# Kernel tuning notes

Measured on AMD Instinct MI355X. Metric: run time of the kernel, lower is better.

## Reference

```python
import jax, jax.numpy as jnp
import numpy as np
import math

ALPHA, BETA = 0.0, 0.1  # MarketRelation defaults


def setup_inputs() -> dict:
    key = jax.random.key(0)
    ks = jax.random.split(key, 15)
    n, T, d, K, C = 1024, 8, 64, 8, 64
    h = d  # hidden = (2*infeat)//2 = infeat
    s = 0.1
    u = jax.random.uniform(ks[13], (n, n, K), jnp.float32, 1e-6, 1.0 - 1e-6)
    return {
        "x":   jax.random.normal(ks[0], (n, T, d), jnp.float32),
        "Ind": jax.random.uniform(ks[1], (n, n), jnp.float32),
        "Loc": jax.random.uniform(ks[2], (n, n), jnp.float32),
        "a":   jax.random.normal(ks[3], (T, 1), jnp.float32),
        "W1m": jax.random.normal(ks[4], (2 * d, h), jnp.float32) * s,
        "b1m": jax.random.normal(ks[5], (h,), jnp.float32) * s,
        "W2m": jax.random.normal(ks[6], (h, 1), jnp.float32) * s,
        "b2m": jax.random.normal(ks[7], (1,), jnp.float32) * s,
        "W1s": jax.random.normal(ks[8], (2 * d, h), jnp.float32) * s,
        "b1s": jax.random.normal(ks[9], (h,), jnp.float32) * s,
        "W2s": jax.random.normal(ks[10], (h, K), jnp.float32) * s,
        "b2s": jax.random.normal(ks[11], (K,), jnp.float32) * s,
        "E":   jax.random.normal(ks[12], (K, n, C), jnp.float32) * s,
        "g":   -jnp.log(-jnp.log(u)),  # Gumbel(0,1) noise for gumbel_softmax
    }


def reference(x, Ind, Loc, a, W1m, b1m, W2m, b2m, W1s, b1s, W2s, b2s, E, g):
    n, T, d = x.shape
    # --- MarketRelation ---
    # fc1(concat(x_j, x_k)) == x_j @ W1m[:d] + x_k @ W1m[d:] + b1m (same math,
    # avoids materializing the N x N x 2d concat tensor)
    W1a, W1b = W1m[:d], W1m[d:]
    a_soft = jax.nn.softmax(a, axis=0)  # [T,1]
    A_mkt = jnp.zeros((n, n), x.dtype)
    for i in range(T):
        xi = x[:, i, :]                      # [n,d]
        hA = xi @ W1a                        # [n,h]
        hB = xi @ W1b                        # [n,h]
        hmat = jax.nn.relu(hA[:, None, :] + hB[None, :, :] + b1m)  # [n,n,h]
        adj = jax.nn.relu(hmat @ W2m + b2m)[..., 0]                # [n,n]
        factor = 1.0 + ALPHA * math.exp(-BETA * (T - i - 1))
        A_mkt = A_mkt + adj * (a_soft[i, 0] * factor)
    # --- NobsRelation (on last timestep) ---
    xl = x[:, -1, :]
    Ws1a, Ws1b = W1s[:d], W1s[d:]
    hs = jax.nn.relu((xl @ Ws1a)[:, None, :] + (xl @ Ws1b)[None, :, :] + b1s)
    logits = jax.nn.relu(hs @ W2s + b2s)          # [n,n,K]
    y = jax.nn.softmax(logits + g, axis=-1)       # gumbel_softmax, tau=1, soft
    D = jnp.einsum('knc,kmc->nmk', E, E)          # stack of E_k E_k^T, [n,n,K]
    A_nobs = jnp.sum(D * y, axis=-1)              # [n,n]
    return jnp.stack([Ind, Loc, A_mkt, A_nobs])   # [4,n,n]
```

## Files before the change

kernel.cpp:

```cpp
#include <hip/hip_runtime.h>

typedef unsigned short USH;
typedef float v2f __attribute__((ext_vector_type(2)));

__device__ __forceinline__ float bf2f(USH u) {
    return __uint_as_float(((unsigned int)u) << 16);
}
__device__ __forceinline__ float lo16(unsigned int u) { return __uint_as_float(u << 16); }
__device__ __forceinline__ float hi16(unsigned int u) { return __uint_as_float(u & 0xFFFF0000u); }
__device__ __forceinline__ USH f2bf(float f) {
    unsigned int i = __float_as_uint(f);
    i += 0x7FFFu + ((i >> 16) & 1u);
    return (USH)(i >> 16);
}
__device__ __forceinline__ v2f relu2(v2f s) {
    return __builtin_elementwise_max(s, (v2f)(0.0f));
}

__device__ __forceinline__ float ldf(const void* p, long idx, int bf) {
    return bf ? bf2f(((const USH*)p)[idx]) : ((const float*)p)[idx];
}
__device__ __forceinline__ void ld4(const void* p, long idx, int bf, float o[4]) {
    if (bf) {
        ushort4 u = *(const ushort4*)((const USH*)p + idx);
        o[0] = bf2f(u.x); o[1] = bf2f(u.y); o[2] = bf2f(u.z); o[3] = bf2f(u.w);
    } else {
        float4 v = *(const float4*)((const float*)p + idx);
        o[0] = v.x; o[1] = v.y; o[2] = v.z; o[3] = v.w;
    }
}

__device__ __forceinline__ int detect_bf(const void* ind) {
    const uint4* p = (const uint4*)ind;
    unsigned o = 0;
    #pragma unroll
    for (int i = 0; i < 8; ++i) { uint4 v = p[i]; o |= v.x | v.y | v.z | v.w; }
    return (o & 0x8000u) == 0;
}


__global__ __launch_bounds__(256) void k_pre_d(
    const void* __restrict__ x,
    const void* __restrict__ W1m,
    const void* __restrict__ b1m,
    const void* __restrict__ W1s,
    const void* __restrict__ b1s,
    const void* __restrict__ E,
    const void* __restrict__ IndDet,
    USH* __restrict__ hA, USH* __restrict__ hBb,
    USH* __restrict__ hsA, USH* __restrict__ hsBb,
    USH* __restrict__ D)
{
    __shared__ float smem[8192];
    float* sA = smem;
    float* sB = smem + 4096;
    const int bf = detect_bf(IndDet);
    const int tid = threadIdx.x;
    const int bid = blockIdx.x;
    const int tx = tid & 15, ty = tid >> 4;

    if (bid < 2048) {
        const int mb = (bid & 15) * 64, nb = ((bid >> 4) & 15) * 64, k = bid >> 8;
        const long ek = (long)k * 65536;
        {
            const int r_l = tid >> 2, cq = tid & 3;
            const long bn = ek + (long)(nb + r_l) * 64 + cq * 16;
            const long bm = ek + (long)(mb + r_l) * 64 + cq * 16;
            #pragma unroll
            for (int j = 0; j < 4; ++j) {
                const int c0 = cq * 16 + j * 4;
                float o[4];
                ld4(E, bn + j * 4, bf, o);
                #pragma unroll
                for (int e = 0; e < 4; ++e) sA[(c0 + e) * 64 + r_l] = o[e];
                ld4(E, bm + j * 4, bf, o);
                #pragma unroll
                for (int e = 0; e < 4; ++e) sB[(c0 + e) * 64 + r_l] = o[e];
            }
        }
        __syncthreads();
        const int m0 = tx * 4, n0 = ty * 4;
        v2f acc2[4][2] = {};
        #pragma unroll 8
        for (int c = 0; c < 64; ++c) {
            const float4 an = *(const float4*)&sA[c * 64 + n0];
            const float4 am = *(const float4*)&sB[c * 64 + m0];
            const float aa[4] = {an.x, an.y, an.z, an.w};
            v2f m01; m01.x = am.x; m01.y = am.y;
            v2f m23; m23.x = am.z; m23.y = am.w;
            #pragma unroll
            for (int ni = 0; ni < 4; ++ni) {
                const v2f av = (v2f)(aa[ni]);
                acc2[ni][0] = __builtin_elementwise_fma(av, m01, acc2[ni][0]);
                acc2[ni][1] = __builtin_elementwise_fma(av, m23, acc2[ni][1]);
            }
        }
        #pragma unroll
        for (int ni = 0; ni < 4; ++ni) {
            ushort4 o;
            o.x = f2bf(acc2[ni][0].x); o.y = f2bf(acc2[ni][0].y);
            o.z = f2bf(acc2[ni][1].x); o.w = f2bf(acc2[ni][1].y);
            *(ushort4*)&D[(long)k * 1048576 + (long)(nb + n0 + ni) * 1024 + mb + m0] = o;
        }
    } else {
        const int bid2 = bid - 2048;
        const int nbase = (bid2 & 15) * 64;
        const int by = bid2 >> 4;
        int t, rb;
        const void* Wsrc;
        const void* bias;
        USH* dst;
        if (by < 8)        { t = by;     rb = 0;  Wsrc = W1m; bias = nullptr; dst = hA + by * 65536; }
        else if (by < 16)  { t = by - 8; rb = 64; Wsrc = W1m; bias = b1m;     dst = hBb + (by - 8) * 65536; }
        else if (by == 16) { t = 7;      rb = 0;  Wsrc = W1s; bias = nullptr; dst = hsA; }
        else               { t = 7;      rb = 64; Wsrc = W1s; bias = b1s;     dst = hsBb; }

        {
            const int n_l = tid >> 2, dq = tid & 3;
            const long base = (long)(nbase + n_l) * 512 + t * 64 + dq * 16;
            #pragma unroll
            for (int j = 0; j < 4; ++j) {
                float o[4]; ld4(x, base + j * 4, bf, o);
                const int d0 = dq * 16 + j * 4;
                #pragma unroll
                for (int e = 0; e < 4; ++e) sA[(d0 + e) * 64 + n_l] = o[e];
            }
        }
        {
            const int d_l = tid >> 2, cq = tid & 3;
            const long base = (long)(rb + d_l) * 64 + cq * 16;
            #pragma unroll
            for (int j = 0; j < 4; ++j) {
                float o[4]; ld4(Wsrc, base + j * 4, bf, o);
                const int c0 = cq * 16 + j * 4;
                #pragma unroll
                for (int e = 0; e < 4; ++e) sB[d_l * 64 + c0 + e] = o[e];
            }
        }
        __syncthreads();

        const int c0 = tx * 4, nq = ty * 4;
        float acc[4][4] = {};
        #pragma unroll 16
        for (int d = 0; d < 64; ++d) {
            const float4 xa = *(const float4*)&sA[d * 64 + nq];
            const float4 wv = *(const float4*)&sB[d * 64 + c0];
            const float aa[4] = {xa.x, xa.y, xa.z, xa.w};
            const float ww[4] = {wv.x, wv.y, wv.z, wv.w};
            #pragma unroll
            for (int ci = 0; ci < 4; ++ci)
                #pragma unroll
                for (int ni = 0; ni < 4; ++ni)
                    acc[ci][ni] += ww[ci] * aa[ni];
        }
        #pragma unroll
        for (int ci = 0; ci < 4; ++ci) {
            const float bb = bias ? ldf(bias, c0 + ci, bf) : 0.0f;
            ushort4 o;
            o.x = f2bf(acc[ci][0] + bb); o.y = f2bf(acc[ci][1] + bb);
            o.z = f2bf(acc[ci][2] + bb); o.w = f2bf(acc[ci][3] + bb);
            *(ushort4*)&dst[(c0 + ci) * 1024 + nbase + nq] = o;
        }
    }
}

__global__ __launch_bounds__(256, 4) void k_main(
    const USH* __restrict__ hA, const USH* __restrict__ hBb,
    const USH* __restrict__ hsA, const USH* __restrict__ hsBb,
    const USH* __restrict__ Dm,
    const void* __restrict__ Ind, const void* __restrict__ Loc,
    const void* __restrict__ a, const void* __restrict__ W2m,
    const void* __restrict__ b2m, const void* __restrict__ W2s,
    const void* __restrict__ b2s, const void* __restrict__ g,
    void* __restrict__ out)
{
    __shared__ float As[2][64 * 32];
    __shared__ float Bs[2][64 * 32];
    __shared__ float w2s_l[64 * 8];
    __shared__ float w2m_l[64];
    __shared__ float asoft_l[8];

    const int bf = detect_bf(Ind);
    const int tid = threadIdx.x;
    const int mb = blockIdx.x * 32, nb = blockIdx.y * 32;
    const int tx = tid & 15, ty = tid >> 4;
    const int m0 = tx * 2, n0 = ty * 2;

    if (tid < 64) w2m_l[tid] = ldf(W2m, tid, bf);
    if (tid >= 64 && tid < 192) {
        const int q = tid - 64;
        float o[4]; ld4(W2s, q * 4, bf, o);
        #pragma unroll
        for (int e = 0; e < 4; ++e) w2s_l[q * 4 + e] = o[e];
    }
    if (tid < 8) {
        float av[8], mx = -1e30f, s = 0.0f;
        #pragma unroll
        for (int k = 0; k < 8; ++k) { av[k] = ldf(a, k, bf); mx = fmaxf(mx, av[k]); }
        #pragma unroll
        for (int k = 0; k < 8; ++k) s += __expf(av[k] - mx);
        asoft_l[tid] = __expf(av[tid] - mx) / s;
    }
    const float b2m_f = ldf(b2m, 0, bf);

    const int offA = (tid >> 2) * 1024 + nb + (tid & 3) * 8;
    const int offB = (tid >> 2) * 1024 + mb + (tid & 3) * 8;
    const int ldsOff = tid * 8;

    {
        const uint4 pa = *(const uint4*)(hA + offA);
        const uint4 pb = *(const uint4*)(hBb + offB);
        float4 fa0, fa1, fb0, fb1;
        fa0.x = lo16(pa.x); fa0.y = hi16(pa.x); fa0.z = lo16(pa.y); fa0.w = hi16(pa.y);
        fa1.x = lo16(pa.z); fa1.y = hi16(pa.z); fa1.z = lo16(pa.w); fa1.w = hi16(pa.w);
        fb0.x = lo16(pb.x); fb0.y = hi16(pb.x); fb0.z = lo16(pb.y); fb0.w = hi16(pb.y);
        fb1.x = lo16(pb.z); fb1.y = hi16(pb.z); fb1.z = lo16(pb.w); fb1.w = hi16(pb.w);
        *(float4*)&As[0][ldsOff] = fa0; *(float4*)&As[0][ldsOff + 4] = fa1;
        *(float4*)&Bs[0][ldsOff] = fb0; *(float4*)&Bs[0][ldsOff + 4] = fb1;
    }
    __syncthreads();

    v2f amk2[2] = {(v2f)(0.0f), (v2f)(0.0f)};

    for (int t = 0; t < 8; ++t) {
        const int cur = t & 1, nxt = cur ^ 1;
        const USH* srcA = (t < 7) ? (hA + (t + 1) * 65536) : hsA;
        const USH* srcB = (t < 7) ? (hBb + (t + 1) * 65536) : hsBb;
        const uint4 pa = *(const uint4*)(srcA + offA);
        const uint4 pb = *(const uint4*)(srcB + offB);

        v2f acc2[2] = {(v2f)(0.0f), (v2f)(0.0f)};
        #pragma unroll
        for (int c4 = 0; c4 < 16; ++c4) {
            const float4 wq = *(const float4*)&w2m_l[c4 * 4];
            const float ww[4] = {wq.x, wq.y, wq.z, wq.w};
            #pragma unroll
            for (int j = 0; j < 4; ++j) {
                const int c = c4 * 4 + j;
                const v2f aa = *(const v2f*)&As[cur][(c << 5) + n0];
                const v2f bb = *(const v2f*)&Bs[cur][(c << 5) + m0];
                const v2f wv = (v2f)(ww[j]);
                const v2f s0 = relu2((v2f)(aa.x) + bb);
                const v2f s1 = relu2((v2f)(aa.y) + bb);
                acc2[0] = __builtin_elementwise_fma(s0, wv, acc2[0]);
                acc2[1] = __builtin_elementwise_fma(s1, wv, acc2[1]);
            }
        }
        const v2f asv = (v2f)(asoft_l[t]);
        const v2f b2v = (v2f)(b2m_f);
        amk2[0] = __builtin_elementwise_fma(relu2(acc2[0] + b2v), asv, amk2[0]);
        amk2[1] = __builtin_elementwise_fma(relu2(acc2[1] + b2v), asv, amk2[1]);

        float4 f0, f1;
        f0.x = lo16(pa.x); f0.y = hi16(pa.x); f0.z = lo16(pa.y); f0.w = hi16(pa.y);
        f1.x = lo16(pa.z); f1.y = hi16(pa.z); f1.z = lo16(pa.w); f1.w = hi16(pa.w);
        *(float4*)&As[nxt][ldsOff] = f0; *(float4*)&As[nxt][ldsOff + 4] = f1;
        f0.x = lo16(pb.x); f0.y = hi16(pb.x); f0.z = lo16(pb.y); f0.w = hi16(pb.y);
        f1.x = lo16(pb.z); f1.y = hi16(pb.z); f1.z = lo16(pb.w); f1.w = hi16(pb.w);
        *(float4*)&Bs[nxt][ldsOff] = f0; *(float4*)&Bs[nxt][ldsOff + 4] = f1;
        __syncthreads();
    }

    v2f lgp[2][8];
    #pragma unroll
    for (int i = 0; i < 2; ++i)
        #pragma unroll
        for (int k = 0; k < 8; ++k) lgp[i][k] = (v2f)(0.0f);

    #pragma unroll 4
    for (int c = 0; c < 64; ++c) {
        const v2f aa = *(const v2f*)&As[0][(c << 5) + n0];
        const v2f bb = *(const v2f*)&Bs[0][(c << 5) + m0];
        const v2f z0 = relu2((v2f)(aa.x) + bb);
        const v2f z1 = relu2((v2f)(aa.y) + bb);
        const float4 wa = *(const float4*)&w2s_l[c << 3];
        const float4 wb = *(const float4*)&w2s_l[(c << 3) + 4];
        const float wk[8] = {wa.x, wa.y, wa.z, wa.w, wb.x, wb.y, wb.z, wb.w};
        #pragma unroll
        for (int k = 0; k < 8; ++k) {
            const v2f wkv = (v2f)(wk[k]);
            lgp[0][k] = __builtin_elementwise_fma(z0, wkv, lgp[0][k]);
            lgp[1][k] = __builtin_elementwise_fma(z1, wkv, lgp[1][k]);
        }
    }

    float b2s_f[8];
    #pragma unroll
    for (int k = 0; k < 8; ++k) b2s_f[k] = ldf(b2s, k, bf);

    #pragma unroll
    for (int i = 0; i < 2; ++i) {
        const long rowoff = (long)(nb + n0 + i) * 1024 + mb + m0;
        float gv[16];
        ld4(g, rowoff * 8 + 0, bf, gv + 0);
        ld4(g, rowoff * 8 + 4, bf, gv + 4);
        ld4(g, rowoff * 8 + 8, bf, gv + 8);
        ld4(g, rowoff * 8 + 12, bf, gv + 12);

        float s0 = 0.0f, s1 = 0.0f, d0 = 0.0f, d1 = 0.0f;
        #pragma unroll
        for (int k = 0; k < 8; ++k) {
            const v2f lr = relu2(lgp[i][k] + (v2f)(b2s_f[k]));
            const float e0 = __expf(lr.x + gv[k]);
            const float e1 = __expf(lr.y + gv[8 + k]);
            s0 += e0; s1 += e1;
            const ushort2 dv = *(const ushort2*)&Dm[((long)k << 20) + rowoff];
            d0 += bf2f(dv.x) * e0;
            d1 += bf2f(dv.y) * e1;
        }

        if (bf) {
            USH* o = (USH*)out;
            *(ushort2*)&o[rowoff] = *(const ushort2*)&((const USH*)Ind)[rowoff];
            *(ushort2*)&o[1048576 + rowoff] = *(const ushort2*)&((const USH*)Loc)[rowoff];
            ushort2 o2; o2.x = f2bf(amk2[i].x); o2.y = f2bf(amk2[i].y);
            *(ushort2*)&o[2 * 1048576 + rowoff] = o2;
            ushort2 o3; o3.x = f2bf(d0 / s0); o3.y = f2bf(d1 / s1);
            *(ushort2*)&o[3 * 1048576 + rowoff] = o3;
        } else {
            float* o = (float*)out;
            *(float2*)&o[rowoff] = *(const float2*)&((const float*)Ind)[rowoff];
            *(float2*)&o[1048576 + rowoff] = *(const float2*)&((const float*)Loc)[rowoff];
            float2 o2; o2.x = amk2[i].x; o2.y = amk2[i].y;
            *(float2*)&o[2 * 1048576 + rowoff] = o2;
            float2 o3; o3.x = d0 / s0; o3.y = d1 / s1;
            *(float2*)&o[3 * 1048576 + rowoff] = o3;
        }
    }
}

extern "C" void kernel_launch(void* const* d_in, const int* in_sizes, int n_in,
                              void* d_out, int out_size, void* d_ws, size_t ws_size,
                              hipStream_t stream) {
    const void* x   = d_in[0];
    const void* Ind = d_in[1];
    const void* Loc = d_in[2];
    const void* a   = d_in[3];
    const void* W1m = d_in[4];
    const void* b1m = d_in[5];
    const void* W2m = d_in[6];
    const void* b2m = d_in[7];
    const void* W1s = d_in[8];
    const void* b1s = d_in[9];
    const void* W2s = d_in[10];
    const void* b2s = d_in[11];
    const void* E   = d_in[12];
    const void* g   = d_in[13];

    USH* ws   = (USH*)d_ws;
    USH* hA   = ws;
    USH* hBb  = hA + 524288;
    USH* hsA  = hBb + 524288;
    USH* hsBb = hsA + 65536;
    USH* Dm   = hsBb + 65536;

    k_pre_d<<<dim3(2336), 256, 0, stream>>>(x, W1m, b1m, W1s, b1s, E, Ind,
                                            hA, hBb, hsA, hsBb, Dm);
    k_main<<<dim3(32, 32), 256, 0, stream>>>(hA, hBb, hsA, hsBb, Dm,
                                             Ind, Loc, a, W2m, b2m, W2s, b2s,
                                             g, d_out);
}
```

Measured before the change: 186.0 us.

## Restructure main kernel: fp32 intermediates, wave-uniform A rows, register W2m

The precomputed hidden projections are now stored as fp32 instead of bf16. hA is laid out row-major per node, so each wave reads its eight n-rows as wave-uniform (scalar/broadcast) loads. hB is stored channel-pair interleaved and staged in LDS, double-buffered across timesteps. The main kernel tile changes to 64 m by 32 n, with each lane owning one m column and eight n rows, and W2m and the softmax weights are held in registers. This removes bf16 unpacking and most LDS traffic for A, but doubles intermediate memory size, raises register pressure (launch bounds drop to 2 blocks per SM), and makes the output stores scalar per element.

```diff
diff --git a/kernel.cpp b/kernel.cpp
--- a/kernel.cpp
+++ b/kernel.cpp
@@ -6,8 +6,6 @@
 __device__ __forceinline__ float bf2f(USH u) {
     return __uint_as_float(((unsigned int)u) << 16);
 }
-__device__ __forceinline__ float lo16(unsigned int u) { return __uint_as_float(u << 16); }
-__device__ __forceinline__ float hi16(unsigned int u) { return __uint_as_float(u & 0xFFFF0000u); }
 __device__ __forceinline__ USH f2bf(float f) {
     unsigned int i = __float_as_uint(f);
     i += 0x7FFFu + ((i >> 16) & 1u);
@@ -47,8 +45,8 @@
     const void* __restrict__ b1s,
     const void* __restrict__ E,
     const void* __restrict__ IndDet,
-    USH* __restrict__ hA, USH* __restrict__ hBb,
-    USH* __restrict__ hsA, USH* __restrict__ hsBb,
+    float* __restrict__ hAf,
+    float* __restrict__ hBf,
     USH* __restrict__ D)
 {
     __shared__ float smem[8192];
@@ -109,11 +107,11 @@
         int t, rb;
         const void* Wsrc;
         const void* bias;
-        USH* dst;
-        if (by < 8)        { t = by;     rb = 0;  Wsrc = W1m; bias = nullptr; dst = hA + by * 65536; }
-        else if (by < 16)  { t = by - 8; rb = 64; Wsrc = W1m; bias = b1m;     dst = hBb + (by - 8) * 65536; }
-        else if (by == 16) { t = 7;      rb = 0;  Wsrc = W1s; bias = nullptr; dst = hsA; }
-        else               { t = 7;      rb = 64; Wsrc = W1s; bias = b1s;     dst = hsBb; }
+        float* dst;
+        if (by < 8)        { t = by;     rb = 0;  Wsrc = W1m; bias = nullptr; dst = hAf + by * 65536; }
+        else if (by < 16)  { t = by - 8; rb = 64; Wsrc = W1m; bias = b1m;     dst = hBf + (by - 8) * 65536; }
+        else if (by == 16) { t = 7;      rb = 0;  Wsrc = W1s; bias = nullptr; dst = hAf + 8 * 65536; }
+        else               { t = 7;      rb = 64; Wsrc = W1s; bias = b1s;     dst = hBf + 8 * 65536; }
 
         {
             const int n_l = tid >> 2, dq = tid & 3;
@@ -153,20 +151,32 @@
                 for (int ni = 0; ni < 4; ++ni)
                     acc[ci][ni] += ww[ci] * aa[ni];
         }
-        #pragma unroll
-        for (int ci = 0; ci < 4; ++ci) {
-            const float bb = bias ? ldf(bias, c0 + ci, bf) : 0.0f;
-            ushort4 o;
-            o.x = f2bf(acc[ci][0] + bb); o.y = f2bf(acc[ci][1] + bb);
-            o.z = f2bf(acc[ci][2] + bb); o.w = f2bf(acc[ci][3] + bb);
-            *(ushort4*)&dst[(c0 + ci) * 1024 + nbase + nq] = o;
-        }
-    }
-}
-
-__global__ __launch_bounds__(256, 4) void k_main(
-    const USH* __restrict__ hA, const USH* __restrict__ hBb,
-    const USH* __restrict__ hsA, const USH* __restrict__ hsBb,
+        if (rb == 0) {
+            #pragma unroll
+            for (int ni = 0; ni < 4; ++ni) {
+                float4 o;
+                o.x = acc[0][ni]; o.y = acc[1][ni]; o.z = acc[2][ni]; o.w = acc[3][ni];
+                *(float4*)&dst[(nbase + nq + ni) * 64 + c0] = o;
+            }
+        } else {
+            float b[4];
+            #pragma unroll
+            for (int ci = 0; ci < 4; ++ci) b[ci] = ldf(bias, c0 + ci, bf);
+            #pragma unroll
+            for (int ni = 0; ni < 4; ++ni) {
+                const int mr = nbase + nq + ni;
+                v2f o0; o0.x = acc[0][ni] + b[0]; o0.y = acc[1][ni] + b[1];
+                v2f o1; o1.x = acc[2][ni] + b[2]; o1.y = acc[3][ni] + b[3];
+                *(v2f*)&dst[(c0 >> 1) * 2048 + mr * 2] = o0;
+                *(v2f*)&dst[((c0 >> 1) + 1) * 2048 + mr * 2] = o1;
+            }
+        }
+    }
+}
+
+__global__ __launch_bounds__(256, 2) void k_main(
+    const float* __restrict__ hAf,
+    const float* __restrict__ hBf,
     const USH* __restrict__ Dm,
     const void* __restrict__ Ind, const void* __restrict__ Loc,
     const void* __restrict__ a, const void* __restrict__ W2m,
@@ -174,157 +184,169 @@
     const void* __restrict__ b2s, const void* __restrict__ g,
     void* __restrict__ out)
 {
-    __shared__ float As[2][64 * 32];
-    __shared__ float Bs[2][64 * 32];
-    __shared__ float w2s_l[64 * 8];
-    __shared__ float w2m_l[64];
-    __shared__ float asoft_l[8];
+    __shared__ float Bs[2][4096];
+    __shared__ float w2s_l[512];
 
     const int bf = detect_bf(Ind);
     const int tid = threadIdx.x;
-    const int mb = blockIdx.x * 32, nb = blockIdx.y * 32;
-    const int tx = tid & 15, ty = tid >> 4;
-    const int m0 = tx * 2, n0 = ty * 2;
-
-    if (tid < 64) w2m_l[tid] = ldf(W2m, tid, bf);
-    if (tid >= 64 && tid < 192) {
-        const int q = tid - 64;
-        float o[4]; ld4(W2s, q * 4, bf, o);
-        #pragma unroll
-        for (int e = 0; e < 4; ++e) w2s_l[q * 4 + e] = o[e];
-    }
-    if (tid < 8) {
+    const int mb = blockIdx.x * 64;
+    const int nb = blockIdx.y * 32;
+    const int lane = tid & 63;
+    const int wid = __builtin_amdgcn_readfirstlane(tid >> 6);
+    const int m = mb + lane;
+    const int scp = tid >> 5;
+    const int sq4 = (tid & 31) << 2;
+
+    #pragma unroll
+    for (int i = 0; i < 4; ++i) {
+        const int cp = i * 8 + scp;
+        const float4 v = *(const float4*)(hBf + cp * 2048 + mb * 2 + sq4);
+        *(float4*)&Bs[0][cp * 128 + sq4] = v;
+    }
+    if (tid < 128) {
+        float o[4];
+        ld4(W2s, tid * 4, bf, o);
+        w2s_l[tid * 4 + 0] = o[0]; w2s_l[tid * 4 + 1] = o[1];
+        w2s_l[tid * 4 + 2] = o[2]; w2s_l[tid * 4 + 3] = o[3];
+    }
+
+    v2f w2mv[32];
+    #pragma unroll
+    for (int q = 0; q < 16; ++q) {
+        float o[4]; ld4(W2m, q * 4, bf, o);
+        v2f u; u.x = o[0]; u.y = o[1]; w2mv[2 * q] = u;
+        v2f w; w.x = o[2]; w.y = o[3]; w2mv[2 * q + 1] = w;
+    }
+    const float b2m_f = ldf(b2m, 0, bf);
+    float asf[8];
+    {
         float av[8], mx = -1e30f, s = 0.0f;
         #pragma unroll
         for (int k = 0; k < 8; ++k) { av[k] = ldf(a, k, bf); mx = fmaxf(mx, av[k]); }
         #pragma unroll
-        for (int k = 0; k < 8; ++k) s += __expf(av[k] - mx);
-        asoft_l[tid] = __expf(av[tid] - mx) / s;
-    }
-    const float b2m_f = ldf(b2m, 0, bf);
-
-    const int offA = (tid >> 2) * 1024 + nb + (tid & 3) * 8;
-    const int offB = (tid >> 2) * 1024 + mb + (tid & 3) * 8;
-    const int ldsOff = tid * 8;
-
-    {
-        const uint4 pa = *(const uint4*)(hA + offA);
-        const uint4 pb = *(const uint4*)(hBb + offB);
-        float4 fa0, fa1, fb0, fb1;
-        fa0.x = lo16(pa.x); fa0.y = hi16(pa.x); fa0.z = lo16(pa.y); fa0.w = hi16(pa.y);
-        fa1.x = lo16(pa.z); fa1.y = hi16(pa.z); fa1.z = lo16(pa.w); fa1.w = hi16(pa.w);
-        fb0.x = lo16(pb.x); fb0.y = hi16(pb.x); fb0.z = lo16(pb.y); fb0.w = hi16(pb.y);
-        fb1.x = lo16(pb.z); fb1.y = hi16(pb.z); fb1.z = lo16(pb.w); fb1.w = hi16(pb.w);
-        *(float4*)&As[0][ldsOff] = fa0; *(float4*)&As[0][ldsOff + 4] = fa1;
-        *(float4*)&Bs[0][ldsOff] = fb0; *(float4*)&Bs[0][ldsOff + 4] = fb1;
+        for (int k = 0; k < 8; ++k) { av[k] = __expf(av[k] - mx); s += av[k]; }
+        #pragma unroll
+        for (int k = 0; k < 8; ++k) asf[k] = av[k] / s;
     }
     __syncthreads();
 
-    v2f amk2[2] = {(v2f)(0.0f), (v2f)(0.0f)};
+    float amk[8] = {0.f, 0.f, 0.f, 0.f, 0.f, 0.f, 0.f, 0.f};
 
     for (int t = 0; t < 8; ++t) {
-        const int cur = t & 1, nxt = cur ^ 1;
-        const USH* srcA = (t < 7) ? (hA + (t + 1) * 65536) : hsA;
-        const USH* srcB = (t < 7) ? (hBb + (t + 1) * 65536) : hsBb;
-        const uint4 pa = *(const uint4*)(srcA + offA);
-        const uint4 pb = *(const uint4*)(srcB + offB);
-
-        v2f acc2[2] = {(v2f)(0.0f), (v2f)(0.0f)};
-        #pragma unroll
-        for (int c4 = 0; c4 < 16; ++c4) {
-            const float4 wq = *(const float4*)&w2m_l[c4 * 4];
-            const float ww[4] = {wq.x, wq.y, wq.z, wq.w};
-            #pragma unroll
-            for (int j = 0; j < 4; ++j) {
-                const int c = c4 * 4 + j;
-                const v2f aa = *(const v2f*)&As[cur][(c << 5) + n0];
-                const v2f bb = *(const v2f*)&Bs[cur][(c << 5) + m0];
-                const v2f wv = (v2f)(ww[j]);
-                const v2f s0 = relu2((v2f)(aa.x) + bb);
-                const v2f s1 = relu2((v2f)(aa.y) + bb);
-                acc2[0] = __builtin_elementwise_fma(s0, wv, acc2[0]);
-                acc2[1] = __builtin_elementwise_fma(s1, wv, acc2[1]);
-            }
-        }
-        const v2f asv = (v2f)(asoft_l[t]);
-        const v2f b2v = (v2f)(b2m_f);
-        amk2[0] = __builtin_elementwise_fma(relu2(acc2[0] + b2v), asv, amk2[0]);
-        amk2[1] = __builtin_elementwise_fma(relu2(acc2[1] + b2v), asv, amk2[1]);
-
-        float4 f0, f1;
-        f0.x = lo16(pa.x); f0.y = hi16(pa.x); f0.z = lo16(pa.y); f0.w = hi16(pa.y);
-        f1.x = lo16(pa.z); f1.y = hi16(pa.z); f1.z = lo16(pa.w); f1.w = hi16(pa.w);
-        *(float4*)&As[nxt][ldsOff] = f0; *(float4*)&As[nxt][ldsOff + 4] = f1;
-        f0.x = lo16(pb.x); f0.y = hi16(pb.x); f0.z = lo16(pb.y); f0.w = hi16(pb.y);
-        f1.x = lo16(pb.z); f1.y = hi16(pb.z); f1.z = lo16(pb.w); f1.w = hi16(pb.w);
-        *(float4*)&Bs[nxt][ldsOff] = f0; *(float4*)&Bs[nxt][ldsOff + 4] = f1;
+        const int cur = t & 1;
+        float4 st[4];
+        #pragma unroll
+        for (int i = 0; i < 4; ++i) {
+            const int cp = i * 8 + scp;
+            st[i] = *(const float4*)(hBf + (t + 1) * 65536 + cp * 2048 + mb * 2 + sq4);
+        }
+
+        v2f acc[8];
+        #pragma unroll
+        for (int ni = 0; ni < 8; ++ni) acc[ni] = (v2f)(0.0f);
+        const float* At = hAf + ((t * 1024) + nb + wid * 8) * 64;
+        #pragma unroll
+        for (int ch = 0; ch < 4; ++ch) {
+            v2f bbv[8];
+            #pragma unroll
+            for (int j = 0; j < 8; ++j)
+                bbv[j] = *(const v2f*)&Bs[cur][(ch * 8 + j) * 128 + lane * 2];
+            #pragma unroll
+            for (int ni = 0; ni < 8; ++ni) {
+                const v2f* Ar = (const v2f*)(At + ni * 64 + ch * 16);
+                #pragma unroll
+                for (int j = 0; j < 8; ++j) {
+                    const v2f s = relu2(bbv[j] + Ar[j]);
+                    acc[ni] = __builtin_elementwise_fma(s, w2mv[ch * 8 + j], acc[ni]);
+                }
+            }
+        }
+        const float as_t = asf[t];
+        #pragma unroll
+        for (int ni = 0; ni < 8; ++ni)
+            amk[ni] += fmaxf(acc[ni].x + acc[ni].y + b2m_f, 0.0f) * as_t;
+
+        #pragma unroll
+        for (int i = 0; i < 4; ++i) {
+            const int cp = i * 8 + scp;
+            *(float4*)&Bs[cur ^ 1][cp * 128 + sq4] = st[i];
+        }
         __syncthreads();
     }
 
-    v2f lgp[2][8];
-    #pragma unroll
-    for (int i = 0; i < 2; ++i)
-        #pragma unroll
-        for (int k = 0; k < 8; ++k) lgp[i][k] = (v2f)(0.0f);
-
-    #pragma unroll 4
-    for (int c = 0; c < 64; ++c) {
-        const v2f aa = *(const v2f*)&As[0][(c << 5) + n0];
-        const v2f bb = *(const v2f*)&Bs[0][(c << 5) + m0];
-        const v2f z0 = relu2((v2f)(aa.x) + bb);
-        const v2f z1 = relu2((v2f)(aa.y) + bb);
-        const float4 wa = *(const float4*)&w2s_l[c << 3];
-        const float4 wb = *(const float4*)&w2s_l[(c << 3) + 4];
-        const float wk[8] = {wa.x, wa.y, wa.z, wa.w, wb.x, wb.y, wb.z, wb.w};
-        #pragma unroll
-        for (int k = 0; k < 8; ++k) {
-            const v2f wkv = (v2f)(wk[k]);
-            lgp[0][k] = __builtin_elementwise_fma(z0, wkv, lgp[0][k]);
-            lgp[1][k] = __builtin_elementwise_fma(z1, wkv, lgp[1][k]);
-        }
-    }
-
-    float b2s_f[8];
-    #pragma unroll
-    for (int k = 0; k < 8; ++k) b2s_f[k] = ldf(b2s, k, bf);
-
-    #pragma unroll
-    for (int i = 0; i < 2; ++i) {
-        const long rowoff = (long)(nb + n0 + i) * 1024 + mb + m0;
-        float gv[16];
-        ld4(g, rowoff * 8 + 0, bf, gv + 0);
+    v2f lg[8][4];
+    #pragma unroll
+    for (int ni = 0; ni < 8; ++ni)
+        #pragma unroll
+        for (int kp = 0; kp < 4; ++kp) lg[ni][kp] = (v2f)(0.0f);
+
+    const float* A8 = hAf + (8 * 1024 + nb + wid * 8) * 64;
+    #pragma unroll
+    for (int ch = 0; ch < 16; ++ch) {
+        const v2f bb0 = *(const v2f*)&Bs[0][(ch * 2 + 0) * 128 + lane * 2];
+        const v2f bb1 = *(const v2f*)&Bs[0][(ch * 2 + 1) * 128 + lane * 2];
+        v2f wsl[4][4];
+        #pragma unroll
+        for (int cc = 0; cc < 4; ++cc) {
+            const float4 wa = *(const float4*)&w2s_l[(ch * 4 + cc) * 8];
+            const float4 wb = *(const float4*)&w2s_l[(ch * 4 + cc) * 8 + 4];
+            wsl[cc][0].x = wa.x; wsl[cc][0].y = wa.y;
+            wsl[cc][1].x = wa.z; wsl[cc][1].y = wa.w;
+            wsl[cc][2].x = wb.x; wsl[cc][2].y = wb.y;
+            wsl[cc][3].x = wb.z; wsl[cc][3].y = wb.w;
+        }
+        #pragma unroll
+        for (int ni = 0; ni < 8; ++ni) {
+            const v2f* Ar = (const v2f*)(A8 + ni * 64 + ch * 4);
+            const v2f s0 = relu2(bb0 + Ar[0]);
+            const v2f s1 = relu2(bb1 + Ar[1]);
+            #pragma unroll
+            for (int kp = 0; kp < 4; ++kp) {
+                lg[ni][kp] = __builtin_elementwise_fma((v2f)(s0.x), wsl[0][kp], lg[ni][kp]);
+                lg[ni][kp] = __builtin_elementwise_fma((v2f)(s0.y), wsl[1][kp], lg[ni][kp]);
+                lg[ni][kp] = __builtin_elementwise_fma((v2f)(s1.x), wsl[2][kp], lg[ni][kp]);
+                lg[ni][kp] = __builtin_elementwise_fma((v2f)(s1.y), wsl[3][kp], lg[ni][kp]);
+            }
+        }
+    }
+
+    v2f b2sv[4];
+    #pragma unroll
+    for (int kp = 0; kp < 4; ++kp) {
+        b2sv[kp].x = ldf(b2s, 2 * kp, bf);
+        b2sv[kp].y = ldf(b2s, 2 * kp + 1, bf);
+    }
+
+    #pragma unroll
+    for (int ni = 0; ni < 8; ++ni) {
+        const int n = nb + wid * 8 + ni;
+        const long rowoff = ((long)n << 10) + m;
+        float gv[8];
+        ld4(g, rowoff * 8, bf, gv);
         ld4(g, rowoff * 8 + 4, bf, gv + 4);
-        ld4(g, rowoff * 8 + 8, bf, gv + 8);
-        ld4(g, rowoff * 8 + 12, bf, gv + 12);
-
-        float s0 = 0.0f, s1 = 0.0f, d0 = 0.0f, d1 = 0.0f;
-        #pragma unroll
-        for (int k = 0; k < 8; ++k) {
-            const v2f lr = relu2(lgp[i][k] + (v2f)(b2s_f[k]));
-            const float e0 = __expf(lr.x + gv[k]);
-            const float e1 = __expf(lr.y + gv[8 + k]);
-            s0 += e0; s1 += e1;
-            const ushort2 dv = *(const ushort2*)&Dm[((long)k << 20) + rowoff];
-            d0 += bf2f(dv.x) * e0;
-            d1 += bf2f(dv.y) * e1;
-        }
-
+        float ssum = 0.0f, dsum = 0.0f;
+        #pragma unroll
+        for (int kp = 0; kp < 4; ++kp) {
+            const v2f lr = relu2(lg[ni][kp] + b2sv[kp]);
+            const float e0 = __expf(lr.x + gv[2 * kp]);
+            const float e1 = __expf(lr.y + gv[2 * kp + 1]);
+            ssum += e0 + e1;
+            dsum += bf2f(Dm[((long)(2 * kp) << 20) + rowoff]) * e0
+                  + bf2f(Dm[((long)(2 * kp + 1) << 20) + rowoff]) * e1;
+        }
+        const float nobs = dsum / ssum;
         if (bf) {
             USH* o = (USH*)out;
-            *(ushort2*)&o[rowoff] = *(const ushort2*)&((const USH*)Ind)[rowoff];
-            *(ushort2*)&o[1048576 + rowoff] = *(const ushort2*)&((const USH*)Loc)[rowoff];
-            ushort2 o2; o2.x = f2bf(amk2[i].x); o2.y = f2bf(amk2[i].y);
-            *(ushort2*)&o[2 * 1048576 + rowoff] = o2;
-            ushort2 o3; o3.x = f2bf(d0 / s0); o3.y = f2bf(d1 / s1);
-            *(ushort2*)&o[3 * 1048576 + rowoff] = o3;
+            o[rowoff] = ((const USH*)Ind)[rowoff];
+            o[1048576 + rowoff] = ((const USH*)Loc)[rowoff];
+            o[2 * 1048576 + rowoff] = f2bf(amk[ni]);
+            o[3 * 1048576 + rowoff] = f2bf(nobs);
         } else {
             float* o = (float*)out;
-            *(float2*)&o[rowoff] = *(const float2*)&((const float*)Ind)[rowoff];
-            *(float2*)&o[1048576 + rowoff] = *(const float2*)&((const float*)Loc)[rowoff];
-            float2 o2; o2.x = amk2[i].x; o2.y = amk2[i].y;
-            *(float2*)&o[2 * 1048576 + rowoff] = o2;
-            float2 o3; o3.x = d0 / s0; o3.y = d1 / s1;
-            *(float2*)&o[3 * 1048576 + rowoff] = o3;
+            o[rowoff] = ((const float*)Ind)[rowoff];
+            o[1048576 + rowoff] = ((const float*)Loc)[rowoff];
+            o[2 * 1048576 + rowoff] = amk[ni];
+            o[3 * 1048576 + rowoff] = nobs;
         }
     }
 }
@@ -347,16 +369,14 @@
     const void* E   = d_in[12];
     const void* g   = d_in[13];
 
-    USH* ws   = (USH*)d_ws;
-    USH* hA   = ws;
-    USH* hBb  = hA + 524288;
-    USH* hsA  = hBb + 524288;
-    USH* hsBb = hsA + 65536;
-    USH* Dm   = hsBb + 65536;
+    float* ws  = (float*)d_ws;
+    float* hAf = ws;
+    float* hBf = hAf + 589824;
+    USH*   Dm  = (USH*)(hBf + 589824);
 
     k_pre_d<<<dim3(2336), 256, 0, stream>>>(x, W1m, b1m, W1s, b1s, E, Ind,
-                                            hA, hBb, hsA, hsBb, Dm);
-    k_main<<<dim3(32, 32), 256, 0, stream>>>(hA, hBb, hsA, hsBb, Dm,
+                                            hAf, hBf, Dm);
+    k_main<<<dim3(16, 32), 256, 0, stream>>>(hAf, hBf, Dm,
                                              Ind, Loc, a, W2m, b2m, W2s, b2s,
                                              g, d_out);
 }
```

Measured after the change: 510.3 us. 2.74x slower.

## Store hidden projections as fp32 and enlarge k_main tile to 64x32

Applied to the files above, without the earlier changes.

The precomputed hidden projections hA/hB are now stored as fp32 instead of bf16, with the NOBS projections packed as a ninth slice. This removes the unpack step in k_main and makes indexing uniform. k_main's per-block tile grows from 32x32 to 64x32, with each thread handling 4 rows instead of 2, so every loaded B value and weight is reused across more outputs. The costs are double the workspace traffic for the projections, more LDS, and higher register pressure, with launch_bounds lowered to 2 blocks per SM.

```diff
diff --git a/kernel.cpp b/kernel.cpp
--- a/kernel.cpp
+++ b/kernel.cpp
@@ -6,8 +6,6 @@
 __device__ __forceinline__ float bf2f(USH u) {
     return __uint_as_float(((unsigned int)u) << 16);
 }
-__device__ __forceinline__ float lo16(unsigned int u) { return __uint_as_float(u << 16); }
-__device__ __forceinline__ float hi16(unsigned int u) { return __uint_as_float(u & 0xFFFF0000u); }
 __device__ __forceinline__ USH f2bf(float f) {
     unsigned int i = __float_as_uint(f);
     i += 0x7FFFu + ((i >> 16) & 1u);
@@ -47,8 +45,8 @@
     const void* __restrict__ b1s,
     const void* __restrict__ E,
     const void* __restrict__ IndDet,
-    USH* __restrict__ hA, USH* __restrict__ hBb,
-    USH* __restrict__ hsA, USH* __restrict__ hsBb,
+    float* __restrict__ hAf,
+    float* __restrict__ hBf,
     USH* __restrict__ D)
 {
     __shared__ float smem[8192];
@@ -109,11 +107,11 @@
         int t, rb;
         const void* Wsrc;
         const void* bias;
-        USH* dst;
-        if (by < 8)        { t = by;     rb = 0;  Wsrc = W1m; bias = nullptr; dst = hA + by * 65536; }
-        else if (by < 16)  { t = by - 8; rb = 64; Wsrc = W1m; bias = b1m;     dst = hBb + (by - 8) * 65536; }
-        else if (by == 16) { t = 7;      rb = 0;  Wsrc = W1s; bias = nullptr; dst = hsA; }
-        else               { t = 7;      rb = 64; Wsrc = W1s; bias = b1s;     dst = hsBb; }
+        float* dst;
+        if (by < 8)        { t = by;     rb = 0;  Wsrc = W1m; bias = nullptr; dst = hAf + by * 65536; }
+        else if (by < 16)  { t = by - 8; rb = 64; Wsrc = W1m; bias = b1m;     dst = hBf + (by - 8) * 65536; }
+        else if (by == 16) { t = 7;      rb = 0;  Wsrc = W1s; bias = nullptr; dst = hAf + 8 * 65536; }
+        else               { t = 7;      rb = 64; Wsrc = W1s; bias = b1s;     dst = hBf + 8 * 65536; }
 
         {
             const int n_l = tid >> 2, dq = tid & 3;
@@ -153,20 +151,24 @@
                 for (int ni = 0; ni < 4; ++ni)
                     acc[ci][ni] += ww[ci] * aa[ni];
         }
+        float b[4] = {0.f, 0.f, 0.f, 0.f};
+        if (bias) {
+            #pragma unroll
+            for (int ci = 0; ci < 4; ++ci) b[ci] = ldf(bias, c0 + ci, bf);
+        }
         #pragma unroll
         for (int ci = 0; ci < 4; ++ci) {
-            const float bb = bias ? ldf(bias, c0 + ci, bf) : 0.0f;
-            ushort4 o;
-            o.x = f2bf(acc[ci][0] + bb); o.y = f2bf(acc[ci][1] + bb);
-            o.z = f2bf(acc[ci][2] + bb); o.w = f2bf(acc[ci][3] + bb);
-            *(ushort4*)&dst[(c0 + ci) * 1024 + nbase + nq] = o;
-        }
-    }
-}
-
-__global__ __launch_bounds__(256, 4) void k_main(
-    const USH* __restrict__ hA, const USH* __restrict__ hBb,
-    const USH* __restrict__ hsA, const USH* __restrict__ hsBb,
+            float4 o;
+            o.x = acc[ci][0] + b[ci]; o.y = acc[ci][1] + b[ci];
+            o.z = acc[ci][2] + b[ci]; o.w = acc[ci][3] + b[ci];
+            *(float4*)&dst[(c0 + ci) * 1024 + nbase + nq] = o;
+        }
+    }
+}
+
+__global__ __launch_bounds__(256, 2) void k_main(
+    const float* __restrict__ hAf,
+    const float* __restrict__ hBf,
     const USH* __restrict__ Dm,
     const void* __restrict__ Ind, const void* __restrict__ Loc,
     const void* __restrict__ a, const void* __restrict__ W2m,
@@ -174,17 +176,21 @@
     const void* __restrict__ b2s, const void* __restrict__ g,
     void* __restrict__ out)
 {
-    __shared__ float As[2][64 * 32];
-    __shared__ float Bs[2][64 * 32];
-    __shared__ float w2s_l[64 * 8];
+    __shared__ float As[2][4096];
+    __shared__ float Bs[2][2048];
+    __shared__ float w2s_l[512];
     __shared__ float w2m_l[64];
     __shared__ float asoft_l[8];
 
     const int bf = detect_bf(Ind);
     const int tid = threadIdx.x;
-    const int mb = blockIdx.x * 32, nb = blockIdx.y * 32;
+    const int mb = blockIdx.x * 32, nb = blockIdx.y * 64;
     const int tx = tid & 15, ty = tid >> 4;
-    const int m0 = tx * 2, n0 = ty * 2;
+    const int n0 = ty * 4;
+    const int m0 = tx * 2;
+
+    const int cA = tid >> 4, qA = (tid & 15) * 4;
+    const int cB = tid >> 3, qB = (tid & 7) * 4;
 
     if (tid < 64) w2m_l[tid] = ldf(W2m, tid, bf);
     if (tid >= 64 && tid < 192) {
@@ -203,94 +209,104 @@
     }
     const float b2m_f = ldf(b2m, 0, bf);
 
-    const int offA = (tid >> 2) * 1024 + nb + (tid & 3) * 8;
-    const int offB = (tid >> 2) * 1024 + mb + (tid & 3) * 8;
-    const int ldsOff = tid * 8;
-
-    {
-        const uint4 pa = *(const uint4*)(hA + offA);
-        const uint4 pb = *(const uint4*)(hBb + offB);
-        float4 fa0, fa1, fb0, fb1;
-        fa0.x = lo16(pa.x); fa0.y = hi16(pa.x); fa0.z = lo16(pa.y); fa0.w = hi16(pa.y);
-        fa1.x = lo16(pa.z); fa1.y = hi16(pa.z); fa1.z = lo16(pa.w); fa1.w = hi16(pa.w);
-        fb0.x = lo16(pb.x); fb0.y = hi16(pb.x); fb0.z = lo16(pb.y); fb0.w = hi16(pb.y);
-        fb1.x = lo16(pb.z); fb1.y = hi16(pb.z); fb1.z = lo16(pb.w); fb1.w = hi16(pb.w);
-        *(float4*)&As[0][ldsOff] = fa0; *(float4*)&As[0][ldsOff + 4] = fa1;
-        *(float4*)&Bs[0][ldsOff] = fb0; *(float4*)&Bs[0][ldsOff + 4] = fb1;
+    #pragma unroll
+    for (int p = 0; p < 4; ++p) {
+        const int c = cA + p * 16;
+        *(float4*)&As[0][c * 64 + qA] = *(const float4*)(hAf + (long)c * 1024 + nb + qA);
+    }
+    #pragma unroll
+    for (int p = 0; p < 2; ++p) {
+        const int c = cB + p * 32;
+        *(float4*)&Bs[0][c * 32 + qB] = *(const float4*)(hBf + (long)c * 1024 + mb + qB);
     }
     __syncthreads();
 
-    v2f amk2[2] = {(v2f)(0.0f), (v2f)(0.0f)};
+    v2f amk[4] = {(v2f)(0.0f), (v2f)(0.0f), (v2f)(0.0f), (v2f)(0.0f)};
 
     for (int t = 0; t < 8; ++t) {
         const int cur = t & 1, nxt = cur ^ 1;
-        const USH* srcA = (t < 7) ? (hA + (t + 1) * 65536) : hsA;
-        const USH* srcB = (t < 7) ? (hBb + (t + 1) * 65536) : hsBb;
-        const uint4 pa = *(const uint4*)(srcA + offA);
-        const uint4 pb = *(const uint4*)(srcB + offB);
-
-        v2f acc2[2] = {(v2f)(0.0f), (v2f)(0.0f)};
-        #pragma unroll
+        const float* srcA = hAf + (long)(t + 1) * 65536;
+        const float* srcB = hBf + (long)(t + 1) * 65536;
+        float4 pfa[4], pfb[2];
+        #pragma unroll
+        for (int p = 0; p < 4; ++p)
+            pfa[p] = *(const float4*)(srcA + (long)(cA + p * 16) * 1024 + nb + qA);
+        #pragma unroll
+        for (int p = 0; p < 2; ++p)
+            pfb[p] = *(const float4*)(srcB + (long)(cB + p * 32) * 1024 + mb + qB);
+
+        v2f acc[4] = {(v2f)(0.0f), (v2f)(0.0f), (v2f)(0.0f), (v2f)(0.0f)};
+        const float* Ac = As[cur];
+        const float* Bc = Bs[cur];
+        #pragma unroll 4
         for (int c4 = 0; c4 < 16; ++c4) {
             const float4 wq = *(const float4*)&w2m_l[c4 * 4];
             const float ww[4] = {wq.x, wq.y, wq.z, wq.w};
             #pragma unroll
             for (int j = 0; j < 4; ++j) {
                 const int c = c4 * 4 + j;
-                const v2f aa = *(const v2f*)&As[cur][(c << 5) + n0];
-                const v2f bb = *(const v2f*)&Bs[cur][(c << 5) + m0];
+                const float4 aq = *(const float4*)&Ac[c * 64 + n0];
+                const v2f bb = *(const v2f*)&Bc[c * 32 + m0];
+                const float aa[4] = {aq.x, aq.y, aq.z, aq.w};
                 const v2f wv = (v2f)(ww[j]);
-                const v2f s0 = relu2((v2f)(aa.x) + bb);
-                const v2f s1 = relu2((v2f)(aa.y) + bb);
-                acc2[0] = __builtin_elementwise_fma(s0, wv, acc2[0]);
-                acc2[1] = __builtin_elementwise_fma(s1, wv, acc2[1]);
+                #pragma unroll
+                for (int ni = 0; ni < 4; ++ni) {
+                    const v2f s = relu2(bb + (v2f)(aa[ni]));
+                    acc[ni] = __builtin_elementwise_fma(s, wv, acc[ni]);
+                }
             }
         }
         const v2f asv = (v2f)(asoft_l[t]);
         const v2f b2v = (v2f)(b2m_f);
-        amk2[0] = __builtin_elementwise_fma(relu2(acc2[0] + b2v), asv, amk2[0]);
-        amk2[1] = __builtin_elementwise_fma(relu2(acc2[1] + b2v), asv, amk2[1]);
-
-        float4 f0, f1;
-        f0.x = lo16(pa.x); f0.y = hi16(pa.x); f0.z = lo16(pa.y); f0.w = hi16(pa.y);
-        f1.x = lo16(pa.z); f1.y = hi16(pa.z); f1.z = lo16(pa.w); f1.w = hi16(pa.w);
-        *(float4*)&As[nxt][ldsOff] = f0; *(float4*)&As[nxt][ldsOff + 4] = f1;
-        f0.x = lo16(pb.x); f0.y = hi16(pb.x); f0.z = lo16(pb.y); f0.w = hi16(pb.y);
-        f1.x = lo16(pb.z); f1.y = hi16(pb.z); f1.z = lo16(pb.w); f1.w = hi16(pb.w);
-        *(float4*)&Bs[nxt][ldsOff] = f0; *(float4*)&Bs[nxt][ldsOff + 4] = f1;
+        #pragma unroll
+        for (int ni = 0; ni < 4; ++ni)
+            amk[ni] = __builtin_elementwise_fma(relu2(acc[ni] + b2v), asv, amk[ni]);
+
+        #pragma unroll
+        for (int p = 0; p < 4; ++p)
+            *(float4*)&As[nxt][(cA + p * 16) * 64 + qA] = pfa[p];
+        #pragma unroll
+        for (int p = 0; p < 2; ++p)
+            *(float4*)&Bs[nxt][(cB + p * 32) * 32 + qB] = pfb[p];
         __syncthreads();
     }
 
-    v2f lgp[2][8];
-    #pragma unroll
-    for (int i = 0; i < 2; ++i)
-        #pragma unroll
-        for (int k = 0; k < 8; ++k) lgp[i][k] = (v2f)(0.0f);
-
-    #pragma unroll 4
-    for (int c = 0; c < 64; ++c) {
-        const v2f aa = *(const v2f*)&As[0][(c << 5) + n0];
-        const v2f bb = *(const v2f*)&Bs[0][(c << 5) + m0];
-        const v2f z0 = relu2((v2f)(aa.x) + bb);
-        const v2f z1 = relu2((v2f)(aa.y) + bb);
-        const float4 wa = *(const float4*)&w2s_l[c << 3];
-        const float4 wb = *(const float4*)&w2s_l[(c << 3) + 4];
-        const float wk[8] = {wa.x, wa.y, wa.z, wa.w, wb.x, wb.y, wb.z, wb.w};
-        #pragma unroll
-        for (int k = 0; k < 8; ++k) {
-            const v2f wkv = (v2f)(wk[k]);
-            lgp[0][k] = __builtin_elementwise_fma(z0, wkv, lgp[0][k]);
-            lgp[1][k] = __builtin_elementwise_fma(z1, wkv, lgp[1][k]);
-        }
-    }
-
-    float b2s_f[8];
-    #pragma unroll
-    for (int k = 0; k < 8; ++k) b2s_f[k] = ldf(b2s, k, bf);
-
-    #pragma unroll
-    for (int i = 0; i < 2; ++i) {
-        const long rowoff = (long)(nb + n0 + i) * 1024 + mb + m0;
+    v2f lgm[4][8];
+    #pragma unroll
+    for (int ni = 0; ni < 4; ++ni)
+        #pragma unroll
+        for (int k = 0; k < 8; ++k) lgm[ni][k] = (v2f)(0.0f);
+
+    #pragma unroll 2
+    for (int c4 = 0; c4 < 16; ++c4) {
+        #pragma unroll
+        for (int j = 0; j < 4; ++j) {
+            const int c = c4 * 4 + j;
+            const float4 aq = *(const float4*)&As[0][c * 64 + n0];
+            const v2f bb = *(const v2f*)&Bs[0][c * 32 + m0];
+            const float aa[4] = {aq.x, aq.y, aq.z, aq.w};
+            const float4 wa = *(const float4*)&w2s_l[c * 8];
+            const float4 wb = *(const float4*)&w2s_l[c * 8 + 4];
+            const float wk[8] = {wa.x, wa.y, wa.z, wa.w, wb.x, wb.y, wb.z, wb.w};
+            #pragma unroll
+            for (int ni = 0; ni < 4; ++ni) {
+                const v2f z = relu2(bb + (v2f)(aa[ni]));
+                #pragma unroll
+                for (int k = 0; k < 8; ++k)
+                    lgm[ni][k] = __builtin_elementwise_fma(z, (v2f)(wk[k]), lgm[ni][k]);
+            }
+        }
+    }
+
+    float b2sv[8];
+    #pragma unroll
+    for (int k = 0; k < 8; ++k) b2sv[k] = ldf(b2s, k, bf);
+
+    const int mg = mb + m0;
+    #pragma unroll
+    for (int ni = 0; ni < 4; ++ni) {
+        const int n = nb + n0 + ni;
+        const long rowoff = ((long)n << 10) + mg;
         float gv[16];
         ld4(g, rowoff * 8 + 0, bf, gv + 0);
         ld4(g, rowoff * 8 + 4, bf, gv + 4);
@@ -300,7 +316,7 @@
         float s0 = 0.0f, s1 = 0.0f, d0 = 0.0f, d1 = 0.0f;
         #pragma unroll
         for (int k = 0; k < 8; ++k) {
-            const v2f lr = relu2(lgp[i][k] + (v2f)(b2s_f[k]));
+            const v2f lr = relu2(lgm[ni][k] + (v2f)(b2sv[k]));
             const float e0 = __expf(lr.x + gv[k]);
             const float e1 = __expf(lr.y + gv[8 + k]);
             s0 += e0; s1 += e1;
@@ -313,7 +329,7 @@
             USH* o = (USH*)out;
             *(ushort2*)&o[rowoff] = *(const ushort2*)&((const USH*)Ind)[rowoff];
             *(ushort2*)&o[1048576 + rowoff] = *(const ushort2*)&((const USH*)Loc)[rowoff];
-            ushort2 o2; o2.x = f2bf(amk2[i].x); o2.y = f2bf(amk2[i].y);
+            ushort2 o2; o2.x = f2bf(amk[ni].x); o2.y = f2bf(amk[ni].y);
             *(ushort2*)&o[2 * 1048576 + rowoff] = o2;
             ushort2 o3; o3.x = f2bf(d0 / s0); o3.y = f2bf(d1 / s1);
             *(ushort2*)&o[3 * 1048576 + rowoff] = o3;
@@ -321,7 +337,7 @@
             float* o = (float*)out;
             *(float2*)&o[rowoff] = *(const float2*)&((const float*)Ind)[rowoff];
             *(float2*)&o[1048576 + rowoff] = *(const float2*)&((const float*)Loc)[rowoff];
-            float2 o2; o2.x = amk2[i].x; o2.y = amk2[i].y;
+            float2 o2; o2.x = amk[ni].x; o2.y = amk[ni].y;
             *(float2*)&o[2 * 1048576 + rowoff] = o2;
             float2 o3; o3.x = d0 / s0; o3.y = d1 / s1;
             *(float2*)&o[3 * 1048576 + rowoff] = o3;
@@ -347,16 +363,14 @@
     const void* E   = d_in[12];
     const void* g   = d_in[13];
 
-    USH* ws   = (USH*)d_ws;
-    USH* hA   = ws;
-    USH* hBb  = hA + 524288;
-    USH* hsA  = hBb + 524288;
-    USH* hsBb = hsA + 65536;
-    USH* Dm   = hsBb + 65536;
+    float* ws  = (float*)d_ws;
+    float* hAf = ws;
+    float* hBf = hAf + 589824;
+    USH*   Dm  = (USH*)(hBf + 589824);
 
     k_pre_d<<<dim3(2336), 256, 0, stream>>>(x, W1m, b1m, W1s, b1s, E, Ind,
-                                            hA, hBb, hsA, hsBb, Dm);
-    k_main<<<dim3(32, 32), 256, 0, stream>>>(hA, hBb, hsA, hsBb, Dm,
+                                            hAf, hBf, Dm);
+    k_main<<<dim3(32, 16), 256, 0, stream>>>(hAf, hBf, Dm,
                                              Ind, Loc, a, W2m, b2m, W2s, b2s,
                                              g, d_out);
 }
```

Result: slower. 193.9 us (+4.2%).

## Compute E_k E_k^T Gram matrices with bf16 MFMA on 128x128 tiles

Applied to the files above, without the earlier changes.

Replaces the scalar FP32 FMA outer-product path that computes D = E_k E_k^T in the precompute kernel with MFMA 16x16x32 bf16 instructions. Each block now covers a 128x128 tile instead of 64x64, and the E rows are staged in LDS as bf16 with an XOR swizzle to avoid bank conflicts. This cuts the grid from 2336 to 800 blocks and should reduce ALU time for the Gram stage. When E arrives as fp32, its inputs are rounded to bf16 before the multiply, and the output stores are scalar 2-byte writes.

```diff
diff --git a/kernel.cpp b/kernel.cpp
--- a/kernel.cpp
+++ b/kernel.cpp
@@ -2,6 +2,8 @@
 
 typedef unsigned short USH;
 typedef float v2f __attribute__((ext_vector_type(2)));
+typedef short bfrag __attribute__((ext_vector_type(8)));
+typedef float f32x4 __attribute__((ext_vector_type(4)));
 
 __device__ __forceinline__ float bf2f(USH u) {
     return __uint_as_float(((unsigned int)u) << 16);
@@ -52,58 +54,90 @@
     USH* __restrict__ D)
 {
     __shared__ float smem[8192];
-    float* sA = smem;
-    float* sB = smem + 4096;
     const int bf = detect_bf(IndDet);
     const int tid = threadIdx.x;
     const int bid = blockIdx.x;
-    const int tx = tid & 15, ty = tid >> 4;
-
-    if (bid < 2048) {
-        const int mb = (bid & 15) * 64, nb = ((bid >> 4) & 15) * 64, k = bid >> 8;
+
+    if (bid < 512) {
+        USH* sE = (USH*)smem;
+        const int k = bid >> 6;
+        const int nb = ((bid >> 3) & 7) * 128, mb = (bid & 7) * 128;
         const long ek = (long)k * 65536;
-        {
-            const int r_l = tid >> 2, cq = tid & 3;
-            const long bn = ek + (long)(nb + r_l) * 64 + cq * 16;
-            const long bm = ek + (long)(mb + r_l) * 64 + cq * 16;
-            #pragma unroll
-            for (int j = 0; j < 4; ++j) {
-                const int c0 = cq * 16 + j * 4;
-                float o[4];
-                ld4(E, bn + j * 4, bf, o);
-                #pragma unroll
-                for (int e = 0; e < 4; ++e) sA[(c0 + e) * 64 + r_l] = o[e];
-                ld4(E, bm + j * 4, bf, o);
-                #pragma unroll
-                for (int e = 0; e < 4; ++e) sB[(c0 + e) * 64 + r_l] = o[e];
+
+        const int row = tid >> 1;
+        const int c0 = (tid & 1) * 32;
+        #pragma unroll
+        for (int side = 0; side < 2; ++side) {
+            const int rbase = side ? mb : nb;
+            USH* sDst = sE + side * 8192;
+            const long gbase = ek + (long)(rbase + row) * 64 + c0;
+            USH tmp[32];
+            if (bf) {
+                #pragma unroll
+                for (int q = 0; q < 4; ++q)
+                    *(uint4*)&tmp[q * 8] = *(const uint4*)((const USH*)E + gbase + q * 8);
+            } else {
+                #pragma unroll
+                for (int q = 0; q < 4; ++q) {
+                    const float4 va = *(const float4*)((const float*)E + gbase + q * 8);
+                    const float4 vb = *(const float4*)((const float*)E + gbase + q * 8 + 4);
+                    tmp[q * 8 + 0] = f2bf(va.x); tmp[q * 8 + 1] = f2bf(va.y);
+                    tmp[q * 8 + 2] = f2bf(va.z); tmp[q * 8 + 3] = f2bf(va.w);
+                    tmp[q * 8 + 4] = f2bf(vb.x); tmp[q * 8 + 5] = f2bf(vb.y);
+                    tmp[q * 8 + 6] = f2bf(vb.z); tmp[q * 8 + 7] = f2bf(vb.w);
+                }
+            }
+            #pragma unroll
+            for (int q = 0; q < 4; ++q) {
+                const int byte = (c0 + q * 8) * 2;
+                const int sw = (row * 128 + (byte ^ ((row & 7) << 4))) >> 1;
+                *(uint4*)&sDst[sw] = *(uint4*)&tmp[q * 8];
             }
         }
         __syncthreads();
-        const int m0 = tx * 4, n0 = ty * 4;
-        v2f acc2[4][2] = {};
-        #pragma unroll 8
-        for (int c = 0; c < 64; ++c) {
-            const float4 an = *(const float4*)&sA[c * 64 + n0];
-            const float4 am = *(const float4*)&sB[c * 64 + m0];
-            const float aa[4] = {an.x, an.y, an.z, an.w};
-            v2f m01; m01.x = am.x; m01.y = am.y;
-            v2f m23; m23.x = am.z; m23.y = am.w;
-            #pragma unroll
-            for (int ni = 0; ni < 4; ++ni) {
-                const v2f av = (v2f)(aa[ni]);
-                acc2[ni][0] = __builtin_elementwise_fma(av, m01, acc2[ni][0]);
-                acc2[ni][1] = __builtin_elementwise_fma(av, m23, acc2[ni][1]);
-            }
-        }
-        #pragma unroll
-        for (int ni = 0; ni < 4; ++ni) {
-            ushort4 o;
-            o.x = f2bf(acc2[ni][0].x); o.y = f2bf(acc2[ni][0].y);
-            o.z = f2bf(acc2[ni][1].x); o.w = f2bf(acc2[ni][1].y);
-            *(ushort4*)&D[(long)k * 1048576 + (long)(nb + n0 + ni) * 1024 + mb + m0] = o;
+
+        const int lane = tid & 63;
+        const int w = tid >> 6;
+        const int wn = (w >> 1) * 64, wm = (w & 1) * 64;
+        const int fr = lane & 15, kg = lane >> 4;
+
+        f32x4 acc[4][4] = {};
+        #pragma unroll
+        for (int ks = 0; ks < 2; ++ks) {
+            const int cb = (ks * 32 + kg * 8) * 2;
+            bfrag af[4], bfv[4];
+            #pragma unroll
+            for (int f = 0; f < 4; ++f) {
+                const int ra = wn + f * 16 + fr;
+                af[f] = *(const bfrag*)&sE[(ra * 128 + (cb ^ ((ra & 7) << 4))) >> 1];
+                const int rb = wm + f * 16 + fr;
+                bfv[f] = *(const bfrag*)&sE[8192 + ((rb * 128 + (cb ^ ((rb & 7) << 4))) >> 1)];
+            }
+            #pragma unroll
+            for (int fn = 0; fn < 4; ++fn)
+                #pragma unroll
+                for (int fm = 0; fm < 4; ++fm)
+                    acc[fn][fm] = __builtin_amdgcn_mfma_f32_16x16x32_bf16(
+                        af[fn], bfv[fm], acc[fn][fm], 0, 0, 0);
+        }
+
+        USH* Dk = D + ((long)k << 20);
+        #pragma unroll
+        for (int fn = 0; fn < 4; ++fn) {
+            const int nrow = nb + wn + fn * 16 + kg * 4;
+            #pragma unroll
+            for (int fm = 0; fm < 4; ++fm) {
+                const int mcol = mb + wm + fm * 16 + fr;
+                #pragma unroll
+                for (int r = 0; r < 4; ++r)
+                    Dk[(long)(nrow + r) * 1024 + mcol] = f2bf(acc[fn][fm][r]);
+            }
         }
     } else {
-        const int bid2 = bid - 2048;
+        float* sA = smem;
+        float* sB = smem + 4096;
+        const int tx = tid & 15, ty = tid >> 4;
+        const int bid2 = bid - 512;
         const int nbase = (bid2 & 15) * 64;
         const int by = bid2 >> 4;
         int t, rb;
@@ -354,8 +388,8 @@
     USH* hsBb = hsA + 65536;
     USH* Dm   = hsBb + 65536;
 
-    k_pre_d<<<dim3(2336), 256, 0, stream>>>(x, W1m, b1m, W1s, b1s, E, Ind,
-                                            hA, hBb, hsA, hsBb, Dm);
+    k_pre_d<<<dim3(800), 256, 0, stream>>>(x, W1m, b1m, W1s, b1s, E, Ind,
+                                           hA, hBb, hsA, hsBb, Dm);
     k_main<<<dim3(32, 32), 256, 0, stream>>>(hA, hBb, hsA, hsBb, Dm,
                                              Ind, Loc, a, W2m, b2m, W2s, b2s,
                                              g, d_out);
```

Result: faster. 179.0 us (-3.8%).
